# Kernel optimization log

Measured on AMD Instinct MI355X. Metric: run time of the kernel, lower is better.

Reference implementation:

```python
import jax, jax.numpy as jnp
import numpy as np

NQ, DEPTH = 4, 2
C64 = jnp.complex64


def _ry(theta):
    # theta: scalar or (B,) -> (...,2,2) complex
    h = theta.astype(jnp.float32) / 2
    c, s = jnp.cos(h).astype(C64), jnp.sin(h).astype(C64)
    return jnp.stack([jnp.stack([c, -s], -1), jnp.stack([s, c], -1)], -2)


def _rot(phi, theta, omega):
    # PennyLane Rot = RZ(omega) @ RY(theta) @ RZ(phi), scalars -> (2,2) complex
    h = theta / 2
    c, s = jnp.cos(h), jnp.sin(h)
    ep = jnp.exp(-0.5j * (phi + omega).astype(C64))
    em = jnp.exp(0.5j * (phi - omega).astype(C64))
    return jnp.array(1.0, C64) * jnp.stack([
        jnp.stack([ep * c, -em * s], -1),
        jnp.stack([jnp.conj(em) * s, jnp.conj(ep) * c], -1)], -2)


def _apply_1q(state, U, wire):
    # state: (B,2,2,2,2); U: (2,2) or (B,2,2)
    s = jnp.moveaxis(state, wire + 1, -1)
    if U.ndim == 2:
        s = jnp.einsum('ij,bklmj->bklmi', U, s)
    else:
        s = jnp.einsum('bij,bklmj->bklmi', U, s)
    return jnp.moveaxis(s, -1, wire + 1)


def _cnot(state, ctrl, tgt):
    s = jnp.moveaxis(state, [ctrl + 1, tgt + 1], [-2, -1])
    s = s.at[..., 1, :].set(s[..., 1, ::-1])
    return jnp.moveaxis(s, [-2, -1], [ctrl + 1, tgt + 1])


def _circuit(x, q_weights):
    B = x.shape[0]
    state = jnp.zeros((B, 2, 2, 2, 2), C64).at[:, 0, 0, 0, 0].set(1.0)
    # angle encoding: RY(x[:, w]) on wire w (batched gates)
    for w in range(NQ):
        state = _apply_1q(state, _ry(x[:, w]), w)
    # variational layers
    for layer in range(DEPTH):
        for w in range(NQ):
            U = _rot(q_weights[layer, w, 0], q_weights[layer, w, 1], q_weights[layer, w, 2])
            state = _apply_1q(state, U, w)
        for w in range(NQ - 1):
            state = _cnot(state, w, w + 1)
        state = _cnot(state, NQ - 1, 0)  # num_qubits > 2 wrap-around
    # expval PauliZ on each wire
    probs = jnp.abs(state) ** 2  # (B,2,2,2,2) float32
    z = jnp.array([1.0, -1.0], jnp.float32)
    outs = [jnp.einsum('bijkl,' + 'ijkl'[w] + '->b', probs, z) for w in range(NQ)]
    return jnp.stack(outs, axis=1).astype(x.dtype)  # (B, 4)


def setup_inputs() -> dict:
    key = jax.random.key(0)
    k1, k2 = jax.random.split(key)
    B = 2_000_000
    x = jax.random.uniform(k1, (B, NQ), jnp.float32, minval=0.0, maxval=np.pi)
    q_weights = jax.random.normal(k2, (DEPTH, NQ, 3), jnp.float32) * 0.01
    return {"x": x, "q_weights": q_weights}


def reference(x, q_weights):
    return _circuit(x, q_weights)
```

## Files before the change

### kernel.cpp

```cpp
#include <hip/hip_runtime.h>

#define NQ 4
#define DEPTH 2
#define BLK 256
#define K 4

typedef float v2f __attribute__((ext_vector_type(2)));
typedef float v4f __attribute__((ext_vector_type(4)));

__device__ __forceinline__ void pk_fma_lo_s(v2f& acc, v2f u, v2f b) {
    asm("v_pk_fma_f32 %0, %1, %2, %0 op_sel:[0,0,0] op_sel_hi:[0,1,1]"
        : "+v"(acc) : "s"(u), "v"(b));
}
__device__ __forceinline__ void pk_fma_hi_s(v2f& acc, v2f u, v2f b) {
    asm("v_pk_fma_f32 %0, %1, %2, %0 op_sel:[1,0,0] op_sel_hi:[1,1,1]"
        : "+v"(acc) : "s"(u), "v"(b));
}
__device__ __forceinline__ v2f pk_mul(v2f a, v2f b) {
    v2f d;
    asm("v_pk_mul_f32 %0, %1, %2" : "=v"(d) : "v"(a), "v"(b));
    return d;
}
__device__ __forceinline__ void pk_fma(v2f& acc, v2f a, v2f b) {
    asm("v_pk_fma_f32 %0, %1, %2, %0" : "+v"(acc) : "v"(a), "v"(b));
}

__device__ __forceinline__ float2 cmul(float2 a, float2 b) {
    return make_float2(a.x * b.x - a.y * b.y, a.x * b.y + a.y * b.x);
}
__device__ __forceinline__ float2 cadd(float2 a, float2 b) {
    return make_float2(a.x + b.x, a.y + b.y);
}

__device__ __forceinline__ void build_u_col(const float* __restrict__ qw, int col,
                                            float2 amp[16]) {
#pragma unroll
    for (int i = 0; i < 16; i++)
        amp[i] = make_float2((i == col) ? 1.f : 0.f, 0.f);

#pragma unroll
    for (int layer = 0; layer < DEPTH; layer++) {
#pragma unroll
        for (int w = 0; w < NQ; w++) {
            const float* g = qw + (layer * NQ + w) * 3;
            float phi = g[0], theta = g[1], omega = g[2];
            float ch, sh, sp, cp, sm, cm;
            __sincosf(0.5f * theta, &sh, &ch);
            __sincosf(-0.5f * (phi + omega), &sp, &cp);
            __sincosf(0.5f * (phi - omega), &sm, &cm);
            float2 U00 = make_float2(cp * ch, sp * ch);
            float2 U01 = make_float2(-cm * sh, -sm * sh);
            float2 U10 = make_float2(cm * sh, -sm * sh);
            float2 U11 = make_float2(cp * ch, -sp * ch);
            const int mask = 8 >> w;
#pragma unroll
            for (int i0 = 0; i0 < 16; i0++) {
                if (i0 & mask) continue;
                const int i1 = i0 | mask;
                float2 a0 = amp[i0], a1 = amp[i1];
                amp[i0] = cadd(cmul(U00, a0), cmul(U01, a1));
                amp[i1] = cadd(cmul(U10, a0), cmul(U11, a1));
            }
        }
#pragma unroll
        for (int c = 0; c < NQ; c++) {
            const int t = (c + 1) & 3;
            const int cmsk = 8 >> c, tmsk = 8 >> t;
#pragma unroll
            for (int i = 0; i < 16; i++) {
                if ((i & cmsk) && !(i & tmsk)) {
                    float2 tmp = amp[i];
                    amp[i] = amp[i | tmsk];
                    amp[i | tmsk] = tmp;
                }
            }
        }
    }
}

__global__ void build_u_kernel(const float* __restrict__ qw, v2f* __restrict__ Ug) {
    const int tid = threadIdx.x;
    if (tid < 16) {
        float2 amp[16];
        build_u_col(qw, tid, amp);
#pragma unroll
        for (int i = 0; i < 16; i++) {
            v2f u; u.x = amp[i].x; u.y = amp[i].y;
            Ug[i * 16 + tid] = u;
        }
    }
}

template <typename UPtr>
__device__ __forceinline__ void vqc_main_body(const float* __restrict__ x,
                                              UPtr U,
                                              float* __restrict__ out, int B) {
    const int tid = threadIdx.x;
    const int base = blockIdx.x * (BLK * K) + tid;

    float4 xv[K];
    bool val[K];
#pragma unroll
    for (int k = 0; k < K; k++) {
        const int b = base + k * BLK;
        val[k] = (b < B);
        xv[k] = val[k] ? ((const float4*)x)[b] : make_float4(0.f, 0.f, 0.f, 0.f);
    }

    const float R = 0.07957747154594767f;
    float a01[K][4], a23[K][4];
#pragma unroll
    for (int k = 0; k < K; k++) {
        float s0 = __builtin_amdgcn_sinf(xv[k].x * R), c0 = __builtin_amdgcn_cosf(xv[k].x * R);
        float s1 = __builtin_amdgcn_sinf(xv[k].y * R), c1 = __builtin_amdgcn_cosf(xv[k].y * R);
        float s2 = __builtin_amdgcn_sinf(xv[k].z * R), c2 = __builtin_amdgcn_cosf(xv[k].z * R);
        float s3 = __builtin_amdgcn_sinf(xv[k].w * R), c3 = __builtin_amdgcn_cosf(xv[k].w * R);
        a01[k][0] = c0 * c1; a01[k][1] = c0 * s1; a01[k][2] = s0 * c1; a01[k][3] = s0 * s1;
        a23[k][0] = c2 * c3; a23[k][1] = c2 * s3; a23[k][2] = s2 * c3; a23[k][3] = s2 * s3;
    }
    v2f a01p[2][4], a23p[2][4];
#pragma unroll
    for (int p = 0; p < 2; p++)
#pragma unroll
        for (int i = 0; i < 4; i++) {
            v2f t0; t0.x = a01[2 * p][i]; t0.y = a01[2 * p + 1][i]; a01p[p][i] = t0;
            v2f t1; t1.x = a23[2 * p][i]; t1.y = a23[2 * p + 1][i]; a23p[p][i] = t1;
        }

    v2f ow[4][2];
#pragma unroll
    for (int w = 0; w < 4; w++)
#pragma unroll
        for (int p = 0; p < 2; p++) ow[w][p] = (v2f)0.f;

#pragma unroll 1
    for (int iq = 0; iq < 4; iq++) {
        v2f accre[4][2], accim[4][2];
#pragma unroll
        for (int ii = 0; ii < 4; ii++)
#pragma unroll
            for (int p = 0; p < 2; p++) { accre[ii][p] = (v2f)0.f; accim[ii][p] = (v2f)0.f; }

#pragma unroll
        for (int j = 0; j < 16; j++) {
            v2f ps0 = pk_mul(a01p[0][j >> 2], a23p[0][j & 3]);
            v2f ps1 = pk_mul(a01p[1][j >> 2], a23p[1][j & 3]);
#pragma unroll
            for (int ii = 0; ii < 4; ii++) {
                const v2f u = U[(iq * 4 + ii) * 16 + j];
                pk_fma_lo_s(accre[ii][0], u, ps0);
                pk_fma_hi_s(accim[ii][0], u, ps0);
                pk_fma_lo_s(accre[ii][1], u, ps1);
                pk_fma_hi_s(accim[ii][1], u, ps1);
            }
        }

#pragma unroll
        for (int p = 0; p < 2; p++) {
            v2f p0 = pk_mul(accre[0][p], accre[0][p]); pk_fma(p0, accim[0][p], accim[0][p]);
            v2f p1 = pk_mul(accre[1][p], accre[1][p]); pk_fma(p1, accim[1][p], accim[1][p]);
            v2f p2 = pk_mul(accre[2][p], accre[2][p]); pk_fma(p2, accim[2][p], accim[2][p]);
            v2f p3 = pk_mul(accre[3][p], accre[3][p]); pk_fma(p3, accim[3][p], accim[3][p]);
            v2f s01 = p0 + p1, d01 = p0 - p1;
            v2f s23 = p2 + p3, d23 = p2 - p3;
            v2f ssum = s01 + s23;
            ow[2][p] += s01 - s23;
            ow[3][p] += d01 + d23;
            if (iq & 2) ow[0][p] -= ssum; else ow[0][p] += ssum;
            if (iq & 1) ow[1][p] -= ssum; else ow[1][p] += ssum;
        }
    }

#pragma unroll
    for (int p = 0; p < 2; p++)
#pragma unroll
        for (int e = 0; e < 2; e++) {
            const int k = 2 * p + e;
            const int b = base + k * BLK;
            if (val[k]) {
                float4 o;
                o.x = (e == 0) ? ow[0][p].x : ow[0][p].y;
                o.y = (e == 0) ? ow[1][p].x : ow[1][p].y;
                o.z = (e == 0) ? ow[2][p].x : ow[2][p].y;
                o.w = (e == 0) ? ow[3][p].x : ow[3][p].y;
                ((float4*)out)[b] = o;
            }
        }
}

__global__ __launch_bounds__(BLK) void vqc_main(const float* __restrict__ x,
                                                const v2f* __restrict__ Ug,
                                                float* __restrict__ out, int B) {
    vqc_main_body(x, Ug, out, B);
}

__global__ void vqc_fused(const float* __restrict__ x, const float* __restrict__ qw,
                          float* __restrict__ out, int B) {
    __shared__ v2f Um[256];
    if (threadIdx.x < 16) {
        float2 amp[16];
        build_u_col(qw, threadIdx.x, amp);
#pragma unroll
        for (int i = 0; i < 16; i++) {
            v2f u; u.x = amp[i].x; u.y = amp[i].y;
            Um[i * 16 + threadIdx.x] = u;
        }
    }
    __syncthreads();
    vqc_main_body(x, (const v2f*)Um, out, B);
}

extern "C" void kernel_launch(void* const* d_in, const int* in_sizes, int n_in,
                              void* d_out, int out_size, void* d_ws, size_t ws_size,
                              hipStream_t stream) {
    const float* x  = (const float*)d_in[0];
    const float* qw = (const float*)d_in[1];
    float* out = (float*)d_out;
    const int B = in_sizes[0] / NQ;
    const int blocks = (B + BLK * K - 1) / (BLK * K);

    if (ws_size >= 256 * sizeof(v2f)) {
        v2f* Ug = (v2f*)d_ws;
        build_u_kernel<<<1, 64, 0, stream>>>(qw, Ug);
        vqc_main<<<blocks, BLK, 0, stream>>>(x, Ug, out, B);
    } else {
        vqc_fused<<<blocks, BLK, 0, stream>>>(x, qw, out, B);
    }
}
```

Before: 107.3 us.

## Precompute product-state amplitudes and load U rows with explicit scalar block loads

Builds all 16 product-state amplitudes once up front instead of recomputing them for every output quarter. The main kernel now fetches each pair of unitary rows with inline-asm s_load_dwordx16 into SGPRs, waits once per pair, and feeds those scalars straight into the packed FMAs. This aims to cut scalar-load overhead and compiler-inserted waits in the inner loop. The cost is more VGPRs held for the precomputed amplitudes and hand-written asm wait handling; the fused fallback path gets a matching restructure.

New measurement: 106.6 us. Within noise of the previous version (-0.7%).

```diff
diff --git a/kernel.cpp b/kernel.cpp
--- a/kernel.cpp
+++ b/kernel.cpp
@@ -5,8 +5,8 @@
 #define BLK 256
 #define K 4
 
-typedef float v2f __attribute__((ext_vector_type(2)));
-typedef float v4f __attribute__((ext_vector_type(4)));
+typedef float v2f  __attribute__((ext_vector_type(2)));
+typedef float v16f __attribute__((ext_vector_type(16)));
 
 __device__ __forceinline__ void pk_fma_lo_s(v2f& acc, v2f u, v2f b) {
     asm("v_pk_fma_f32 %0, %1, %2, %0 op_sel:[0,0,0] op_sel_hi:[0,1,1]"
@@ -23,6 +23,18 @@
 }
 __device__ __forceinline__ void pk_fma(v2f& acc, v2f a, v2f b) {
     asm("v_pk_fma_f32 %0, %1, %2, %0" : "+v"(acc) : "v"(a), "v"(b));
+}
+
+__device__ __forceinline__ void sload_row(const v2f* p, v16f& lo, v16f& hi) {
+    asm volatile("s_load_dwordx16 %0, %2, 0x0\n\t"
+                 "s_load_dwordx16 %1, %2, 0x40"
+                 : "=s"(lo), "=s"(hi) : "s"(p) : "memory");
+}
+__device__ __forceinline__ void swait4(v16f& a, v16f& b, v16f& c, v16f& d) {
+    asm volatile("s_waitcnt lgkmcnt(0)" : "+s"(a), "+s"(b), "+s"(c), "+s"(d));
+}
+__device__ __forceinline__ v2f sg_pair(const v16f& r, int q) {
+    v2f u; u.x = r[2 * q]; u.y = r[2 * q + 1]; return u;
 }
 
 __device__ __forceinline__ float2 cmul(float2 a, float2 b) {
@@ -91,22 +103,15 @@
     }
 }
 
-template <typename UPtr>
-__device__ __forceinline__ void vqc_main_body(const float* __restrict__ x,
-                                              UPtr U,
-                                              float* __restrict__ out, int B) {
-    const int tid = threadIdx.x;
-    const int base = blockIdx.x * (BLK * K) + tid;
-
+__device__ __forceinline__ void build_ps(const float* __restrict__ x, int base, int B,
+                                         v2f ps[2][16], bool val[K]) {
     float4 xv[K];
-    bool val[K];
 #pragma unroll
     for (int k = 0; k < K; k++) {
         const int b = base + k * BLK;
         val[k] = (b < B);
         xv[k] = val[k] ? ((const float4*)x)[b] : make_float4(0.f, 0.f, 0.f, 0.f);
     }
-
     const float R = 0.07957747154594767f;
     float a01[K][4], a23[K][4];
 #pragma unroll
@@ -118,59 +123,18 @@
         a01[k][0] = c0 * c1; a01[k][1] = c0 * s1; a01[k][2] = s0 * c1; a01[k][3] = s0 * s1;
         a23[k][0] = c2 * c3; a23[k][1] = c2 * s3; a23[k][2] = s2 * c3; a23[k][3] = s2 * s3;
     }
-    v2f a01p[2][4], a23p[2][4];
 #pragma unroll
     for (int p = 0; p < 2; p++)
 #pragma unroll
-        for (int i = 0; i < 4; i++) {
-            v2f t0; t0.x = a01[2 * p][i]; t0.y = a01[2 * p + 1][i]; a01p[p][i] = t0;
-            v2f t1; t1.x = a23[2 * p][i]; t1.y = a23[2 * p + 1][i]; a23p[p][i] = t1;
-        }
-
-    v2f ow[4][2];
-#pragma unroll
-    for (int w = 0; w < 4; w++)
-#pragma unroll
-        for (int p = 0; p < 2; p++) ow[w][p] = (v2f)0.f;
-
-#pragma unroll 1
-    for (int iq = 0; iq < 4; iq++) {
-        v2f accre[4][2], accim[4][2];
-#pragma unroll
-        for (int ii = 0; ii < 4; ii++)
-#pragma unroll
-            for (int p = 0; p < 2; p++) { accre[ii][p] = (v2f)0.f; accim[ii][p] = (v2f)0.f; }
-
-#pragma unroll
         for (int j = 0; j < 16; j++) {
-            v2f ps0 = pk_mul(a01p[0][j >> 2], a23p[0][j & 3]);
-            v2f ps1 = pk_mul(a01p[1][j >> 2], a23p[1][j & 3]);
-#pragma unroll
-            for (int ii = 0; ii < 4; ii++) {
-                const v2f u = U[(iq * 4 + ii) * 16 + j];
-                pk_fma_lo_s(accre[ii][0], u, ps0);
-                pk_fma_hi_s(accim[ii][0], u, ps0);
-                pk_fma_lo_s(accre[ii][1], u, ps1);
-                pk_fma_hi_s(accim[ii][1], u, ps1);
-            }
-        }
-
-#pragma unroll
-        for (int p = 0; p < 2; p++) {
-            v2f p0 = pk_mul(accre[0][p], accre[0][p]); pk_fma(p0, accim[0][p], accim[0][p]);
-            v2f p1 = pk_mul(accre[1][p], accre[1][p]); pk_fma(p1, accim[1][p], accim[1][p]);
-            v2f p2 = pk_mul(accre[2][p], accre[2][p]); pk_fma(p2, accim[2][p], accim[2][p]);
-            v2f p3 = pk_mul(accre[3][p], accre[3][p]); pk_fma(p3, accim[3][p], accim[3][p]);
-            v2f s01 = p0 + p1, d01 = p0 - p1;
-            v2f s23 = p2 + p3, d23 = p2 - p3;
-            v2f ssum = s01 + s23;
-            ow[2][p] += s01 - s23;
-            ow[3][p] += d01 + d23;
-            if (iq & 2) ow[0][p] -= ssum; else ow[0][p] += ssum;
-            if (iq & 1) ow[1][p] -= ssum; else ow[1][p] += ssum;
-        }
-    }
-
+            v2f t0; t0.x = a01[2 * p][j >> 2]; t0.y = a01[2 * p + 1][j >> 2];
+            v2f t1; t1.x = a23[2 * p][j & 3]; t1.y = a23[2 * p + 1][j & 3];
+            ps[p][j] = pk_mul(t0, t1);
+        }
+}
+
+__device__ __forceinline__ void store_out(float* __restrict__ out, int base, int B,
+                                          const bool val[K], v2f ow[4][2]) {
 #pragma unroll
     for (int p = 0; p < 2; p++)
 #pragma unroll
@@ -191,7 +155,71 @@
 __global__ __launch_bounds__(BLK) void vqc_main(const float* __restrict__ x,
                                                 const v2f* __restrict__ Ug,
                                                 float* __restrict__ out, int B) {
-    vqc_main_body(x, Ug, out, B);
+    const int tid = threadIdx.x;
+    const int base = blockIdx.x * (BLK * K) + tid;
+
+    v2f ps[2][16];
+    bool val[K];
+    build_ps(x, base, B, ps, val);
+
+    v2f ow[4][2];
+#pragma unroll
+    for (int w = 0; w < 4; w++)
+#pragma unroll
+        for (int p = 0; p < 2; p++) ow[w][p] = (v2f)0.f;
+
+#pragma unroll 1
+    for (int iq = 0; iq < 4; iq++) {
+        v2f P[4][2];
+#pragma unroll
+        for (int t = 0; t < 2; t++) {
+            const int r0 = iq * 4 + t * 2;
+            v16f alo, ahi, blo, bhi;
+            sload_row(Ug + r0 * 16, alo, ahi);
+            sload_row(Ug + (r0 + 1) * 16, blo, bhi);
+            swait4(alo, ahi, blo, bhi);
+
+            v2f are[2], aim[2], bre[2], bim[2];
+#pragma unroll
+            for (int p = 0; p < 2; p++) {
+                are[p] = (v2f)0.f; aim[p] = (v2f)0.f;
+                bre[p] = (v2f)0.f; bim[p] = (v2f)0.f;
+            }
+#pragma unroll
+            for (int j = 0; j < 16; j++) {
+                const v2f ua = sg_pair((j < 8) ? alo : ahi, j & 7);
+                const v2f ub = sg_pair((j < 8) ? blo : bhi, j & 7);
+#pragma unroll
+                for (int p = 0; p < 2; p++) {
+                    pk_fma_lo_s(are[p], ua, ps[p][j]);
+                    pk_fma_hi_s(aim[p], ua, ps[p][j]);
+                    pk_fma_lo_s(bre[p], ub, ps[p][j]);
+                    pk_fma_hi_s(bim[p], ub, ps[p][j]);
+                }
+            }
+#pragma unroll
+            for (int p = 0; p < 2; p++) {
+                v2f pa = pk_mul(are[p], are[p]); pk_fma(pa, aim[p], aim[p]);
+                v2f pb = pk_mul(bre[p], bre[p]); pk_fma(pb, bim[p], bim[p]);
+                P[t * 2][p] = pa;
+                P[t * 2 + 1][p] = pb;
+            }
+        }
+
+#pragma unroll
+        for (int p = 0; p < 2; p++) {
+            v2f p0 = P[0][p], p1 = P[1][p], p2 = P[2][p], p3 = P[3][p];
+            v2f s01 = p0 + p1, d01 = p0 - p1;
+            v2f s23 = p2 + p3, d23 = p2 - p3;
+            v2f ssum = s01 + s23;
+            ow[2][p] += s01 - s23;
+            ow[3][p] += d01 + d23;
+            if (iq & 2) ow[0][p] -= ssum; else ow[0][p] += ssum;
+            if (iq & 1) ow[1][p] -= ssum; else ow[1][p] += ssum;
+        }
+    }
+
+    store_out(out, base, B, val, ow);
 }
 
 __global__ void vqc_fused(const float* __restrict__ x, const float* __restrict__ qw,
@@ -207,7 +235,55 @@
         }
     }
     __syncthreads();
-    vqc_main_body(x, (const v2f*)Um, out, B);
+
+    const int tid = threadIdx.x;
+    const int base = blockIdx.x * (BLK * K) + tid;
+    v2f ps[2][16];
+    bool val[K];
+    build_ps(x, base, B, ps, val);
+
+    v2f ow[4][2];
+#pragma unroll
+    for (int w = 0; w < 4; w++)
+#pragma unroll
+        for (int p = 0; p < 2; p++) ow[w][p] = (v2f)0.f;
+
+#pragma unroll 1
+    for (int iq = 0; iq < 4; iq++) {
+        v2f P[4][2];
+#pragma unroll
+        for (int ii = 0; ii < 4; ii++) {
+            v2f re[2] = {(v2f)0.f, (v2f)0.f}, im[2] = {(v2f)0.f, (v2f)0.f};
+#pragma unroll
+            for (int j = 0; j < 16; j++) {
+                const v2f u = Um[(iq * 4 + ii) * 16 + j];
+#pragma unroll
+                for (int p = 0; p < 2; p++) {
+                    v2f ur; ur.x = u.x; ur.y = u.x;
+                    v2f ui; ui.x = u.y; ui.y = u.y;
+                    pk_fma(re[p], ur, ps[p][j]);
+                    pk_fma(im[p], ui, ps[p][j]);
+                }
+            }
+#pragma unroll
+            for (int p = 0; p < 2; p++) {
+                v2f pr = pk_mul(re[p], re[p]); pk_fma(pr, im[p], im[p]);
+                P[ii][p] = pr;
+            }
+        }
+#pragma unroll
+        for (int p = 0; p < 2; p++) {
+            v2f p0 = P[0][p], p1 = P[1][p], p2 = P[2][p], p3 = P[3][p];
+            v2f s01 = p0 + p1, d01 = p0 - p1;
+            v2f s23 = p2 + p3, d23 = p2 - p3;
+            v2f ssum = s01 + s23;
+            ow[2][p] += s01 - s23;
+            ow[3][p] += d01 + d23;
+            if (iq & 2) ow[0][p] -= ssum; else ow[0][p] += ssum;
+            if (iq & 1) ow[1][p] -= ssum; else ow[1][p] += ssum;
+        }
+    }
+    store_out(out, base, B, val, ow);
 }
 
 extern "C" void kernel_launch(void* const* d_in, const int* in_sizes, int n_in,
```
